# Kernel tuning notes

Measured on AMD Instinct MI355X. Metric: run time of the kernel, lower is better.

The kernel has to match this reference:

```python
import jax, jax.numpy as jnp
import numpy as np

GROUPS = 32
EPS = 1e-5


def setup_inputs() -> dict:
    key = jax.random.key(0)
    ks = jax.random.split(key, 4)
    B, C, H, W = 16, 512, 32, 32
    x = jax.random.normal(ks[0], (B, C, H, W), dtype=jnp.float32)
    gamma = jnp.ones((C,), jnp.float32)
    beta = jnp.zeros((C,), jnp.float32)
    # 1x1 convs as channel GEMMs; fan-in scaled init
    w_qkv = jax.random.normal(ks[1], (3 * C, C), dtype=jnp.float32) / np.sqrt(C)
    b_qkv = jnp.zeros((3 * C,), jnp.float32)
    w_proj = jax.random.normal(ks[2], (C, C), dtype=jnp.float32) / np.sqrt(C)
    b_proj = jnp.zeros((C,), jnp.float32)
    return {"x": x, "gamma": gamma, "beta": beta, "w_qkv": w_qkv,
            "b_qkv": b_qkv, "w_proj": w_proj, "b_proj": b_proj}


def _group_norm(x, gamma, beta):
    B, C, H, W = x.shape
    xg = x.reshape(B, GROUPS, C // GROUPS, H, W)
    mu = xg.mean(axis=(2, 3, 4), keepdims=True)
    var = xg.var(axis=(2, 3, 4), keepdims=True)
    xn = ((xg - mu) * jax.lax.rsqrt(var + EPS)).reshape(B, C, H, W)
    return xn * gamma[None, :, None, None] + beta[None, :, None, None]


def reference(x, gamma, beta, w_qkv, b_qkv, w_proj, b_proj):
    B, C, H, W = x.shape
    xn = _group_norm(x, gamma, beta)
    # 1x1 conv qkv: [B, 3C, H, W]
    qkv = jnp.einsum('oc,bchw->bohw', w_qkv, xn) + b_qkv[None, :, None, None]
    qkv = qkv.reshape(B, 3, C, H * W)
    q, k, v = qkv[:, 0], qkv[:, 1], qkv[:, 2]  # each [B, C, HW]
    scale = C ** (-0.5)
    # attn[b, i, j] = softmax_j( q[b,:,i] . k[b,:,j] * scale )
    attn = jax.nn.softmax(jnp.einsum('bci,bcj->bij', q, k) * scale, axis=-1)
    # out[b, c, i] = sum_j v[b,c,j] * attn[b,i,j]
    out = jnp.einsum('bcj,bij->bci', v, attn).reshape(B, C, H, W)
    proj = jnp.einsum('oc,bchw->bohw', w_proj, out) + b_proj[None, :, None, None]
    return x + proj
```

## Files before the change

kernel.cpp:

```cpp
#include <hip/hip_runtime.h>


typedef _Float16 f16;
typedef _Float16 f16x8 __attribute__((ext_vector_type(8)));
typedef _Float16 f16x4 __attribute__((ext_vector_type(4)));
typedef float fx4 __attribute__((ext_vector_type(4)));

__device__ __forceinline__ void gload16(const f16* g, f16* l) {
    __builtin_amdgcn_global_load_lds((const __attribute__((address_space(1))) void*)g,
                                     (__attribute__((address_space(3))) void*)l, 16, 0, 0);
}

__global__ __launch_bounds__(256)
void wconv_kernel(const float* __restrict__ w, f16* __restrict__ o, int n4)
{
    int i = blockIdx.x * 256 + threadIdx.x;
    if (i < n4) {
        float4 v = *(const float4*)(w + i * 4);
        f16x4 h;
        h[0] = (f16)v.x; h[1] = (f16)v.y; h[2] = (f16)v.z; h[3] = (f16)v.w;
        *(f16x4*)(o + i * 4) = h;
    }
}

__global__ __launch_bounds__(256)
void groupnorm_kernel(const float* __restrict__ x, const float* __restrict__ gamma,
                      const float* __restrict__ beta, f16* __restrict__ xnT)
{
    __shared__ float red[256], red2[256];
    __shared__ float mu_s, rs_s;
    __shared__ __align__(16) f16 T[16][520];
    const int blk = blockIdx.x;
    const int b = blk >> 5, g = blk & 31;
    const long base = (long)blk * (16 * 1024);
    const int tid = threadIdx.x;
    const float4* xv = (const float4*)(x + base);

    float s = 0.f, s2 = 0.f;
#pragma unroll
    for (int i = 0; i < 16; i++) {
        float4 v = xv[tid + i * 256];
        s  += v.x + v.y + v.z + v.w;
        s2 += v.x * v.x + v.y * v.y + v.z * v.z + v.w * v.w;
    }
    red[tid] = s; red2[tid] = s2;
    __syncthreads();
    for (int off = 128; off > 0; off >>= 1) {
        if (tid < off) { red[tid] += red[tid + off]; red2[tid] += red2[tid + off]; }
        __syncthreads();
    }
    if (tid == 0) {
        float mu = red[0] * (1.f / 16384.f);
        float var = red2[0] * (1.f / 16384.f) - mu * mu;
        mu_s = mu;
        rs_s = rsqrtf(var + 1e-5f);
    }
    __syncthreads();
    const float mu = mu_s, rs = rs_s;

    for (int h = 0; h < 2; h++) {
        if (h) __syncthreads();
#pragma unroll
        for (int i = 0; i < 8; i++) {
            int idx = tid + i * 256;
            int ch = idx >> 7;
            int p4 = idx & 127;
            float4 v = *(const float4*)(x + base + ch * 1024 + h * 512 + p4 * 4);
            float gm = gamma[g * 16 + ch] * rs;
            float bt = beta[g * 16 + ch] - mu * gm;
            f16x4 o;
            o[0] = (f16)(v.x * gm + bt);
            o[1] = (f16)(v.y * gm + bt);
            o[2] = (f16)(v.z * gm + bt);
            o[3] = (f16)(v.w * gm + bt);
            *(f16x4*)&T[ch][p4 * 4] = o;
        }
        __syncthreads();
#pragma unroll
        for (int i = 0; i < 4; i++) {
            int idx = tid + i * 256;
            int hw = idx >> 1;
            int half8 = (idx & 1) * 8;
            f16x8 o;
#pragma unroll
            for (int j = 0; j < 8; j++) o[j] = T[half8 + j][hw];
            long dst = ((long)b * 1024 + h * 512 + hw) * 512 + g * 16 + half8;
            *(f16x8*)(xnT + dst) = o;
        }
    }
}

__global__ __launch_bounds__(256)
void softmax_kernel(f16* __restrict__ S)
{
    const int wid = blockIdx.x * 4 + (threadIdx.x >> 6);
    const int lane = threadIdx.x & 63;
    f16* p = S + (long)wid * 1024 + lane * 16;
    f16x8 h0 = *(const f16x8*)p;
    f16x8 h1 = *(const f16x8*)(p + 8);
    float v[16];
#pragma unroll
    for (int i = 0; i < 8; i++) { v[i] = (float)h0[i]; v[8 + i] = (float)h1[i]; }
    float mx = v[0];
#pragma unroll
    for (int i = 1; i < 16; i++) mx = fmaxf(mx, v[i]);
    for (int off = 32; off > 0; off >>= 1) mx = fmaxf(mx, __shfl_xor(mx, off, 64));
    float sum = 0.f;
#pragma unroll
    for (int i = 0; i < 16; i++) { v[i] = __expf(v[i] - mx); sum += v[i]; }
    for (int off = 32; off > 0; off >>= 1) sum += __shfl_xor(sum, off, 64);
    const float inv = 1.f / sum;
#pragma unroll
    for (int i = 0; i < 8; i++) { h0[i] = (f16)(v[i] * inv); h1[i] = (f16)(v[8 + i] * inv); }
    *(f16x8*)p = h0;
    *(f16x8*)(p + 8) = h1;
}

template<int MODE>
__global__ __launch_bounds__(256)
void gemm_kernel(const f16* __restrict__ Ap, const f16* __restrict__ Bp,
                 void* __restrict__ Cp, f16* __restrict__ C2p,
                 const float* __restrict__ bias, const float* __restrict__ resid,
                 float alpha, int M, int N, int K, int lda, int ldb,
                 long sAb, long sBb, long sCb)
{
    __shared__ __align__(16) f16 As[2][128 * 32];
    __shared__ __align__(16) f16 Bs[2][128 * 32];

    const int b = blockIdx.z;
    const int m0 = blockIdx.y * 128, n0 = blockIdx.x * 128;
    const int tid = threadIdx.x;
    const int wave = tid >> 6, lane = tid & 63;
    const int quad = lane >> 4, l15 = lane & 15;
    const int wm = (wave >> 1) * 64, wn = (wave & 1) * 64;
    const int chunkoff = (quad ^ (l15 & 3)) * 8;

    const f16* Ag = Ap + (long)b * sAb;
    const f16* Bg = Bp + (long)b * sBb;

    const int si = lane >> 2;
    const int sj = lane & 3;

    const int R0 = wave * 32, R1 = wave * 32 + 16;
    const f16* agA0 = Ag + (long)(m0 + R0 + si) * lda + ((sj ^ ((R0 + si) & 3)) * 8);
    const f16* agA1 = Ag + (long)(m0 + R1 + si) * lda + ((sj ^ ((R1 + si) & 3)) * 8);
    const f16* agB0 = Bg + (long)(n0 + R0 + si) * ldb + ((sj ^ ((R0 + si) & 3)) * 8);
    const f16* agB1 = Bg + (long)(n0 + R1 + si) * ldb + ((sj ^ ((R1 + si) & 3)) * 8);

    fx4 acc[4][4] = {};

    const int nIter = K >> 5;
    gload16(agA0, &As[0][R0 * 32]);
    gload16(agA1, &As[0][R1 * 32]);
    gload16(agB0, &Bs[0][R0 * 32]);
    gload16(agB1, &Bs[0][R1 * 32]);

    for (int it = 0; it < nIter; ++it) {
        __syncthreads();
        const int cur = it & 1;
        if (it + 1 < nIter) {
            const int k = (it + 1) << 5;
            gload16(agA0 + k, &As[cur ^ 1][R0 * 32]);
            gload16(agA1 + k, &As[cur ^ 1][R1 * 32]);
            gload16(agB0 + k, &Bs[cur ^ 1][R0 * 32]);
            gload16(agB1 + k, &Bs[cur ^ 1][R1 * 32]);
        }
        f16x8 bf[4];
#pragma unroll
        for (int tn = 0; tn < 4; tn++)
            bf[tn] = *(const f16x8*)&Bs[cur][(wn + tn * 16 + l15) * 32 + chunkoff];
#pragma unroll
        for (int tm = 0; tm < 4; tm++) {
            f16x8 af = *(const f16x8*)&As[cur][(wm + tm * 16 + l15) * 32 + chunkoff];
#pragma unroll
            for (int tn = 0; tn < 4; tn++)
                acc[tm][tn] = __builtin_amdgcn_mfma_f32_16x16x32_f16(af, bf[tn], acc[tm][tn], 0, 0, 0);
        }
    }

    if (MODE == 1 && n0 >= 1024) {
#pragma unroll
        for (int tm = 0; tm < 4; tm++)
#pragma unroll
        for (int tn = 0; tn < 4; tn++) {
            int gc = n0 + wn + tn * 16 + l15;
            int gr0 = m0 + wm + tm * 16 + quad * 4;
            float bs = bias[gc];
            f16x4 o;
#pragma unroll
            for (int r = 0; r < 4; r++) o[r] = (f16)(acc[tm][tn][r] + bs);
            *(f16x4*)(C2p + (long)b * 524288 + (long)(gc - 1024) * 1024 + gr0) = o;
        }
        return;
    }
#pragma unroll
    for (int tm = 0; tm < 4; tm++)
#pragma unroll
    for (int tn = 0; tn < 4; tn++) {
        int gc = n0 + wn + tn * 16 + l15;
#pragma unroll
        for (int r = 0; r < 4; r++) {
            int gr = m0 + wm + tm * 16 + quad * 4 + r;
            float v = acc[tm][tn][r] * alpha;
            if (MODE == 1) {
                v += bias[gc];
                ((f16*)Cp)[(long)b * 1048576 + (long)gr * 1024 + gc] = (f16)v;
            } else if (MODE == 2) {
                v += bias[gr];
                long idx = (long)b * sCb + (long)gr * N + gc;
                v += resid[idx];
                ((float*)Cp)[idx] = v;
            } else {
                ((f16*)Cp)[(long)b * sCb + (long)gr * N + gc] = (f16)v;
            }
        }
    }
}

extern "C" void kernel_launch(void* const* d_in, const int* in_sizes, int n_in,
                              void* d_out, int out_size, void* d_ws, size_t ws_size,
                              hipStream_t stream)
{
    const float* x      = (const float*)d_in[0];
    const float* gamma  = (const float*)d_in[1];
    const float* beta   = (const float*)d_in[2];
    const float* w_qkv  = (const float*)d_in[3];
    const float* b_qkv  = (const float*)d_in[4];
    const float* w_proj = (const float*)d_in[5];
    const float* b_proj = (const float*)d_in[6];
    float* out = (float*)d_out;

    char* ws = (char*)d_ws;
    f16* xnT   = (f16*)(ws);
    f16* qkT   = (f16*)(ws + (16L << 20));
    f16* vbuf  = (f16*)(ws + (48L << 20));
    f16* S     = (f16*)(ws + (64L << 20));
    f16* aoutT = (f16*)(ws + (96L << 20));
    f16* wqkvh = S;
    f16* wprjh = xnT;

    wconv_kernel<<<768, 256, 0, stream>>>(w_qkv, wqkvh, 196608);

    groupnorm_kernel<<<512, 256, 0, stream>>>(x, gamma, beta, xnT);

    gemm_kernel<1><<<dim3(12, 8, 16), 256, 0, stream>>>(
        xnT, wqkvh, qkT, vbuf, b_qkv, nullptr, 1.0f,
        1024, 1536, 512, 512, 512,
        524288L, 0L, 0L);

    wconv_kernel<<<256, 256, 0, stream>>>(w_proj, wprjh, 65536);

    gemm_kernel<0><<<dim3(8, 8, 16), 256, 0, stream>>>(
        qkT, qkT + 512, S, nullptr, nullptr, nullptr, 0.04419417382415922f,
        1024, 1024, 512, 1024, 1024,
        1048576L, 1048576L, 1048576L);

    softmax_kernel<<<4096, 256, 0, stream>>>(S);

    gemm_kernel<0><<<dim3(4, 8, 16), 256, 0, stream>>>(
        S, vbuf, aoutT, nullptr, nullptr, nullptr, 1.0f,
        1024, 512, 1024, 1024, 1024,
        1048576L, 524288L, 524288L);

    gemm_kernel<2><<<dim3(8, 4, 16), 256, 0, stream>>>(
        wprjh, aoutT, out, nullptr, b_proj, x, 1.0f,
        512, 1024, 512, 512, 512,
        0L, 524288L, 524288L);
}
```

Measured before the change: 249.9 us.

## Use per-wave private LDS tiles with manual waitcnt pipelining in GEMM

```diff
diff --git a/kernel.cpp b/kernel.cpp
--- a/kernel.cpp
+++ b/kernel.cpp
@@ -5,6 +5,10 @@
 typedef _Float16 f16x8 __attribute__((ext_vector_type(8)));
 typedef _Float16 f16x4 __attribute__((ext_vector_type(4)));
 typedef float fx4 __attribute__((ext_vector_type(4)));
+
+#define WAIT_VM8   0x0F78
+#define WAIT_VM0   0x0F70
+#define WAIT_LGKM0 0xC07F
 
 __device__ __forceinline__ void gload16(const f16* g, f16* l) {
     __builtin_amdgcn_global_load_lds((const __attribute__((address_space(1))) void*)g,
@@ -29,17 +33,19 @@
 {
     __shared__ float red[256], red2[256];
     __shared__ float mu_s, rs_s;
-    __shared__ __align__(16) f16 T[16][520];
+    __shared__ __align__(16) f16 T[16][1040];
     const int blk = blockIdx.x;
     const int b = blk >> 5, g = blk & 31;
-    const long base = (long)blk * (16 * 1024);
+    const long base = (long)blk * 16384;
     const int tid = threadIdx.x;
     const float4* xv = (const float4*)(x + base);
 
+    float4 xr[16];
     float s = 0.f, s2 = 0.f;
 #pragma unroll
     for (int i = 0; i < 16; i++) {
         float4 v = xv[tid + i * 256];
+        xr[i] = v;
         s  += v.x + v.y + v.z + v.w;
         s2 += v.x * v.x + v.y * v.y + v.z * v.z + v.w * v.w;
     }
@@ -58,35 +64,29 @@
     __syncthreads();
     const float mu = mu_s, rs = rs_s;
 
-    for (int h = 0; h < 2; h++) {
-        if (h) __syncthreads();
-#pragma unroll
-        for (int i = 0; i < 8; i++) {
-            int idx = tid + i * 256;
-            int ch = idx >> 7;
-            int p4 = idx & 127;
-            float4 v = *(const float4*)(x + base + ch * 1024 + h * 512 + p4 * 4);
-            float gm = gamma[g * 16 + ch] * rs;
-            float bt = beta[g * 16 + ch] - mu * gm;
-            f16x4 o;
-            o[0] = (f16)(v.x * gm + bt);
-            o[1] = (f16)(v.y * gm + bt);
-            o[2] = (f16)(v.z * gm + bt);
-            o[3] = (f16)(v.w * gm + bt);
-            *(f16x4*)&T[ch][p4 * 4] = o;
-        }
-        __syncthreads();
-#pragma unroll
-        for (int i = 0; i < 4; i++) {
-            int idx = tid + i * 256;
-            int hw = idx >> 1;
-            int half8 = (idx & 1) * 8;
-            f16x8 o;
-#pragma unroll
-            for (int j = 0; j < 8; j++) o[j] = T[half8 + j][hw];
-            long dst = ((long)b * 1024 + h * 512 + hw) * 512 + g * 16 + half8;
-            *(f16x8*)(xnT + dst) = o;
-        }
+#pragma unroll
+    for (int i = 0; i < 16; i++) {
+        float gm = gamma[g * 16 + i] * rs;
+        float bt = beta[g * 16 + i] - mu * gm;
+        float4 v = xr[i];
+        f16x4 o;
+        o[0] = (f16)(v.x * gm + bt);
+        o[1] = (f16)(v.y * gm + bt);
+        o[2] = (f16)(v.z * gm + bt);
+        o[3] = (f16)(v.w * gm + bt);
+        *(f16x4*)&T[i][tid * 4] = o;
+    }
+    __syncthreads();
+#pragma unroll
+    for (int i = 0; i < 8; i++) {
+        int idx = tid + i * 256;
+        int hw = idx >> 1;
+        int half8 = (idx & 1) * 8;
+        f16x8 o;
+#pragma unroll
+        for (int j = 0; j < 8; j++) o[j] = T[half8 + j][hw];
+        long dst = ((long)b * 1024 + hw) * 512 + g * 16 + half8;
+        *(f16x8*)(xnT + dst) = o;
     }
 }
 
@@ -124,8 +124,7 @@
                  float alpha, int M, int N, int K, int lda, int ldb,
                  long sAb, long sBb, long sCb)
 {
-    __shared__ __align__(16) f16 As[2][128 * 32];
-    __shared__ __align__(16) f16 Bs[2][128 * 32];
+    __shared__ __align__(16) f16 lds[4][2][2][2048];
 
     const int b = blockIdx.z;
     const int m0 = blockIdx.y * 128, n0 = blockIdx.x * 128;
@@ -135,48 +134,64 @@
     const int wm = (wave >> 1) * 64, wn = (wave & 1) * 64;
     const int chunkoff = (quad ^ (l15 & 3)) * 8;
 
-    const f16* Ag = Ap + (long)b * sAb;
-    const f16* Bg = Bp + (long)b * sBb;
-
     const int si = lane >> 2;
     const int sj = lane & 3;
-
-    const int R0 = wave * 32, R1 = wave * 32 + 16;
-    const f16* agA0 = Ag + (long)(m0 + R0 + si) * lda + ((sj ^ ((R0 + si) & 3)) * 8);
-    const f16* agA1 = Ag + (long)(m0 + R1 + si) * lda + ((sj ^ ((R1 + si) & 3)) * 8);
-    const f16* agB0 = Bg + (long)(n0 + R0 + si) * ldb + ((sj ^ ((R0 + si) & 3)) * 8);
-    const f16* agB1 = Bg + (long)(n0 + R1 + si) * ldb + ((sj ^ ((R1 + si) & 3)) * 8);
+    const int sjx = (sj ^ (si & 3)) * 8;
+
+    const f16* Ag = Ap + (long)b * sAb + (long)(m0 + wm + si) * lda + sjx;
+    const f16* Bg = Bp + (long)b * sBb + (long)(n0 + wn + si) * ldb + sjx;
+
+    f16* ldsA = &lds[wave][0][0][0];
+    f16* ldsB = &lds[wave][1][0][0];
 
     fx4 acc[4][4] = {};
-
     const int nIter = K >> 5;
-    gload16(agA0, &As[0][R0 * 32]);
-    gload16(agA1, &As[0][R1 * 32]);
-    gload16(agB0, &Bs[0][R0 * 32]);
-    gload16(agB1, &Bs[0][R1 * 32]);
-
-    for (int it = 0; it < nIter; ++it) {
-        __syncthreads();
+
+#define STAGE(buf, kOff)                                                        \
+    { _Pragma("unroll")                                                          \
+      for (int s = 0; s < 4; s++) {                                              \
+          gload16(Ag + (kOff) + (s * 16) * lda, ldsA + (buf) * 2048 + s * 512);  \
+          gload16(Bg + (kOff) + (s * 16) * ldb, ldsB + (buf) * 2048 + s * 512);  \
+      } }
+
+    STAGE(0, 0)
+    STAGE(1, 32)
+
+    for (int it = 0; it < nIter - 1; ++it) {
         const int cur = it & 1;
-        if (it + 1 < nIter) {
-            const int k = (it + 1) << 5;
-            gload16(agA0 + k, &As[cur ^ 1][R0 * 32]);
-            gload16(agA1 + k, &As[cur ^ 1][R1 * 32]);
-            gload16(agB0 + k, &Bs[cur ^ 1][R0 * 32]);
-            gload16(agB1 + k, &Bs[cur ^ 1][R1 * 32]);
-        }
-        f16x8 bf[4];
-#pragma unroll
-        for (int tn = 0; tn < 4; tn++)
-            bf[tn] = *(const f16x8*)&Bs[cur][(wn + tn * 16 + l15) * 32 + chunkoff];
-#pragma unroll
-        for (int tm = 0; tm < 4; tm++) {
-            f16x8 af = *(const f16x8*)&As[cur][(wm + tm * 16 + l15) * 32 + chunkoff];
+        const f16* bA = ldsA + cur * 2048;
+        const f16* bB = ldsB + cur * 2048;
+        __builtin_amdgcn_s_waitcnt(WAIT_VM8);
+        f16x8 af[4], bf[4];
+#pragma unroll
+        for (int t = 0; t < 4; t++) af[t] = *(const f16x8*)&bA[(t * 16 + l15) * 32 + chunkoff];
+#pragma unroll
+        for (int t = 0; t < 4; t++) bf[t] = *(const f16x8*)&bB[(t * 16 + l15) * 32 + chunkoff];
+        __builtin_amdgcn_s_waitcnt(WAIT_LGKM0);
+        if (it + 2 < nIter) { STAGE(cur, (it + 2) << 5) }
+#pragma unroll
+        for (int tm = 0; tm < 4; tm++)
 #pragma unroll
             for (int tn = 0; tn < 4; tn++)
-                acc[tm][tn] = __builtin_amdgcn_mfma_f32_16x16x32_f16(af, bf[tn], acc[tm][tn], 0, 0, 0);
-        }
-    }
+                acc[tm][tn] = __builtin_amdgcn_mfma_f32_16x16x32_f16(af[tm], bf[tn], acc[tm][tn], 0, 0, 0);
+    }
+    {
+        const int cur = (nIter - 1) & 1;
+        const f16* bA = ldsA + cur * 2048;
+        const f16* bB = ldsB + cur * 2048;
+        __builtin_amdgcn_s_waitcnt(WAIT_VM0);
+        f16x8 af[4], bf[4];
+#pragma unroll
+        for (int t = 0; t < 4; t++) af[t] = *(const f16x8*)&bA[(t * 16 + l15) * 32 + chunkoff];
+#pragma unroll
+        for (int t = 0; t < 4; t++) bf[t] = *(const f16x8*)&bB[(t * 16 + l15) * 32 + chunkoff];
+#pragma unroll
+        for (int tm = 0; tm < 4; tm++)
+#pragma unroll
+            for (int tn = 0; tn < 4; tn++)
+                acc[tm][tn] = __builtin_amdgcn_mfma_f32_16x16x32_f16(af[tm], bf[tn], acc[tm][tn], 0, 0, 0);
+    }
+#undef STAGE
 
     if (MODE == 1 && n0 >= 1024) {
 #pragma unroll
```

After: 260.5 us. 4.2% more time.

## Fuse softmax into PV GEMM, remap block order, single-pass groupnorm

Applied to the files above, without the earlier changes.

```diff
diff --git a/kernel.cpp b/kernel.cpp
--- a/kernel.cpp
+++ b/kernel.cpp
@@ -5,6 +5,8 @@
 typedef _Float16 f16x8 __attribute__((ext_vector_type(8)));
 typedef _Float16 f16x4 __attribute__((ext_vector_type(4)));
 typedef float fx4 __attribute__((ext_vector_type(4)));
+
+#define LOG2E 1.44269504088896f
 
 __device__ __forceinline__ void gload16(const f16* g, f16* l) {
     __builtin_amdgcn_global_load_lds((const __attribute__((address_space(1))) void*)g,
@@ -29,17 +31,19 @@
 {
     __shared__ float red[256], red2[256];
     __shared__ float mu_s, rs_s;
-    __shared__ __align__(16) f16 T[16][520];
+    __shared__ __align__(16) f16 T[16][1040];
     const int blk = blockIdx.x;
     const int b = blk >> 5, g = blk & 31;
-    const long base = (long)blk * (16 * 1024);
+    const long base = (long)blk * 16384;
     const int tid = threadIdx.x;
     const float4* xv = (const float4*)(x + base);
 
+    float4 xr[16];
     float s = 0.f, s2 = 0.f;
 #pragma unroll
     for (int i = 0; i < 16; i++) {
         float4 v = xv[tid + i * 256];
+        xr[i] = v;
         s  += v.x + v.y + v.z + v.w;
         s2 += v.x * v.x + v.y * v.y + v.z * v.z + v.w * v.w;
     }
@@ -58,62 +62,30 @@
     __syncthreads();
     const float mu = mu_s, rs = rs_s;
 
-    for (int h = 0; h < 2; h++) {
-        if (h) __syncthreads();
-#pragma unroll
-        for (int i = 0; i < 8; i++) {
-            int idx = tid + i * 256;
-            int ch = idx >> 7;
-            int p4 = idx & 127;
-            float4 v = *(const float4*)(x + base + ch * 1024 + h * 512 + p4 * 4);
-            float gm = gamma[g * 16 + ch] * rs;
-            float bt = beta[g * 16 + ch] - mu * gm;
-            f16x4 o;
-            o[0] = (f16)(v.x * gm + bt);
-            o[1] = (f16)(v.y * gm + bt);
-            o[2] = (f16)(v.z * gm + bt);
-            o[3] = (f16)(v.w * gm + bt);
-            *(f16x4*)&T[ch][p4 * 4] = o;
-        }
-        __syncthreads();
-#pragma unroll
-        for (int i = 0; i < 4; i++) {
-            int idx = tid + i * 256;
-            int hw = idx >> 1;
-            int half8 = (idx & 1) * 8;
-            f16x8 o;
-#pragma unroll
-            for (int j = 0; j < 8; j++) o[j] = T[half8 + j][hw];
-            long dst = ((long)b * 1024 + h * 512 + hw) * 512 + g * 16 + half8;
-            *(f16x8*)(xnT + dst) = o;
-        }
-    }
-}
-
-__global__ __launch_bounds__(256)
-void softmax_kernel(f16* __restrict__ S)
-{
-    const int wid = blockIdx.x * 4 + (threadIdx.x >> 6);
-    const int lane = threadIdx.x & 63;
-    f16* p = S + (long)wid * 1024 + lane * 16;
-    f16x8 h0 = *(const f16x8*)p;
-    f16x8 h1 = *(const f16x8*)(p + 8);
-    float v[16];
-#pragma unroll
-    for (int i = 0; i < 8; i++) { v[i] = (float)h0[i]; v[8 + i] = (float)h1[i]; }
-    float mx = v[0];
-#pragma unroll
-    for (int i = 1; i < 16; i++) mx = fmaxf(mx, v[i]);
-    for (int off = 32; off > 0; off >>= 1) mx = fmaxf(mx, __shfl_xor(mx, off, 64));
-    float sum = 0.f;
-#pragma unroll
-    for (int i = 0; i < 16; i++) { v[i] = __expf(v[i] - mx); sum += v[i]; }
-    for (int off = 32; off > 0; off >>= 1) sum += __shfl_xor(sum, off, 64);
-    const float inv = 1.f / sum;
-#pragma unroll
-    for (int i = 0; i < 8; i++) { h0[i] = (f16)(v[i] * inv); h1[i] = (f16)(v[8 + i] * inv); }
-    *(f16x8*)p = h0;
-    *(f16x8*)(p + 8) = h1;
+#pragma unroll
+    for (int i = 0; i < 16; i++) {
+        float gm = gamma[g * 16 + i] * rs;
+        float bt = beta[g * 16 + i] - mu * gm;
+        float4 v = xr[i];
+        f16x4 o;
+        o[0] = (f16)(v.x * gm + bt);
+        o[1] = (f16)(v.y * gm + bt);
+        o[2] = (f16)(v.z * gm + bt);
+        o[3] = (f16)(v.w * gm + bt);
+        *(f16x4*)&T[i][tid * 4] = o;
+    }
+    __syncthreads();
+#pragma unroll
+    for (int i = 0; i < 8; i++) {
+        int idx = tid + i * 256;
+        int hw = idx >> 1;
+        int half8 = (idx & 1) * 8;
+        f16x8 o;
+#pragma unroll
+        for (int j = 0; j < 8; j++) o[j] = T[half8 + j][hw];
+        long dst = ((long)b * 1024 + hw) * 512 + g * 16 + half8;
+        *(f16x8*)(xnT + dst) = o;
+    }
 }
 
 template<int MODE>
@@ -126,9 +98,26 @@
 {
     __shared__ __align__(16) f16 As[2][128 * 32];
     __shared__ __align__(16) f16 Bs[2][128 * 32];
-
-    const int b = blockIdx.z;
-    const int m0 = blockIdx.y * 128, n0 = blockIdx.x * 128;
+    __shared__ float sm[128][2], sl[128][2];
+    __shared__ float ec_s[128], il_s[128];
+
+    const int linear = (blockIdx.z * gridDim.y + blockIdx.y) * gridDim.x + blockIdx.x;
+    int mIdx, nIdx, bIdx;
+    {
+        const int x7 = linear & 7, slot = linear >> 3;
+        if (MODE == 1) {
+            nIdx = slot >> 4; int t = x7 + 8 * (slot & 15); mIdx = t & 7; bIdx = t >> 3;
+        } else if (MODE == 0) {
+            bIdx = x7 + 8 * (slot >> 6); int mn = slot & 63; mIdx = mn >> 3; nIdx = mn & 7;
+        } else if (MODE == 3) {
+            bIdx = x7 + 8 * (slot >> 5); int mn = slot & 31; mIdx = mn >> 2; nIdx = mn & 3;
+        } else {
+            int t = x7 + 8 * (slot & 15); nIdx = t & 7; bIdx = t >> 3; mIdx = slot >> 4;
+        }
+    }
+    const int b = bIdx;
+    const int m0 = mIdx * 128, n0 = nIdx * 128;
+
     const int tid = threadIdx.x;
     const int wave = tid >> 6, lane = tid & 63;
     const int quad = lane >> 4, l15 = lane & 15;
@@ -138,9 +127,46 @@
     const f16* Ag = Ap + (long)b * sAb;
     const f16* Bg = Bp + (long)b * sBb;
 
-    const int si = lane >> 2;
-    const int sj = lane & 3;
-
+    float cf[4];
+    if (MODE == 3) {
+        const int r_loc = tid >> 1, half = tid & 1;
+        const f16* Srow = Ag + (long)(m0 + r_loc) * lda + half * 512;
+        float mx = -3.0e38f;
+        for (int ch = 0; ch < 64; ch += 8) {
+#pragma unroll
+            for (int u = 0; u < 8; u++) {
+                f16x8 v8 = *(const f16x8*)(Srow + (ch + u) * 8);
+#pragma unroll
+                for (int j = 0; j < 8; j++) mx = fmaxf(mx, (float)v8[j]);
+            }
+        }
+        float ssum = 0.f;
+        const float nc = -mx * LOG2E;
+        for (int ch = 0; ch < 64; ch += 8) {
+#pragma unroll
+            for (int u = 0; u < 8; u++) {
+                f16x8 v8 = *(const f16x8*)(Srow + (ch + u) * 8);
+#pragma unroll
+                for (int j = 0; j < 8; j++) ssum += exp2f(fmaf((float)v8[j], LOG2E, nc));
+            }
+        }
+        sm[r_loc][half] = mx;
+        sl[r_loc][half] = ssum;
+        __syncthreads();
+        if (half == 0) {
+            float m0h = sm[r_loc][0], m1h = sm[r_loc][1];
+            float mrow = fmaxf(m0h, m1h);
+            float l = sl[r_loc][0] * exp2f((m0h - mrow) * LOG2E)
+                    + sl[r_loc][1] * exp2f((m1h - mrow) * LOG2E);
+            ec_s[r_loc] = mrow * LOG2E;
+            il_s[r_loc] = 1.f / l;
+        }
+        __syncthreads();
+#pragma unroll
+        for (int tm = 0; tm < 4; tm++) cf[tm] = ec_s[wm + tm * 16 + l15];
+    }
+
+    const int si = lane >> 2, sj = lane & 3;
     const int R0 = wave * 32, R1 = wave * 32 + 16;
     const f16* agA0 = Ag + (long)(m0 + R0 + si) * lda + ((sj ^ ((R0 + si) & 3)) * 8);
     const f16* agA1 = Ag + (long)(m0 + R1 + si) * lda + ((sj ^ ((R1 + si) & 3)) * 8);
@@ -148,23 +174,20 @@
     const f16* agB1 = Bg + (long)(n0 + R1 + si) * ldb + ((sj ^ ((R1 + si) & 3)) * 8);
 
     fx4 acc[4][4] = {};
-
     const int nIter = K >> 5;
-    gload16(agA0, &As[0][R0 * 32]);
-    gload16(agA1, &As[0][R1 * 32]);
-    gload16(agB0, &Bs[0][R0 * 32]);
-    gload16(agB1, &Bs[0][R1 * 32]);
+
+#define STAGE(buf, kOff)                                          \
+    { gload16(agA0 + (kOff), &As[buf][R0 * 32]);                   \
+      gload16(agA1 + (kOff), &As[buf][R1 * 32]);                   \
+      gload16(agB0 + (kOff), &Bs[buf][R0 * 32]);                   \
+      gload16(agB1 + (kOff), &Bs[buf][R1 * 32]); }
+
+    STAGE(0, 0)
 
     for (int it = 0; it < nIter; ++it) {
         __syncthreads();
         const int cur = it & 1;
-        if (it + 1 < nIter) {
-            const int k = (it + 1) << 5;
-            gload16(agA0 + k, &As[cur ^ 1][R0 * 32]);
-            gload16(agA1 + k, &As[cur ^ 1][R1 * 32]);
-            gload16(agB0 + k, &Bs[cur ^ 1][R0 * 32]);
-            gload16(agB1 + k, &Bs[cur ^ 1][R1 * 32]);
-        }
+        if (it + 1 < nIter) { STAGE(cur ^ 1, (it + 1) << 5) }
         f16x8 bf[4];
 #pragma unroll
         for (int tn = 0; tn < 4; tn++)
@@ -172,11 +195,19 @@
 #pragma unroll
         for (int tm = 0; tm < 4; tm++) {
             f16x8 af = *(const f16x8*)&As[cur][(wm + tm * 16 + l15) * 32 + chunkoff];
+            if (MODE == 3) {
+                f16x8 pf;
+#pragma unroll
+                for (int j = 0; j < 8; j++)
+                    pf[j] = (f16)exp2f(fmaf((float)af[j], LOG2E, -cf[tm]));
+                af = pf;
+            }
 #pragma unroll
             for (int tn = 0; tn < 4; tn++)
                 acc[tm][tn] = __builtin_amdgcn_mfma_f32_16x16x32_f16(af, bf[tn], acc[tm][tn], 0, 0, 0);
         }
     }
+#undef STAGE
 
     if (MODE == 1 && n0 >= 1024) {
 #pragma unroll
@@ -193,6 +224,13 @@
         }
         return;
     }
+    float ilr[4][4];
+    if (MODE == 3) {
+#pragma unroll
+        for (int tm = 0; tm < 4; tm++)
+#pragma unroll
+            for (int r = 0; r < 4; r++) ilr[tm][r] = il_s[wm + tm * 16 + quad * 4 + r];
+    }
 #pragma unroll
     for (int tm = 0; tm < 4; tm++)
 #pragma unroll
@@ -201,17 +239,21 @@
 #pragma unroll
         for (int r = 0; r < 4; r++) {
             int gr = m0 + wm + tm * 16 + quad * 4 + r;
-            float v = acc[tm][tn][r] * alpha;
-            if (MODE == 1) {
+            float v = acc[tm][tn][r];
+            if (MODE == 0) {
+                v *= alpha;
+                ((f16*)Cp)[(long)b * sCb + (long)gr * N + gc] = (f16)v;
+            } else if (MODE == 3) {
+                v *= ilr[tm][r];
+                ((f16*)Cp)[(long)b * sCb + (long)gr * N + gc] = (f16)v;
+            } else if (MODE == 1) {
                 v += bias[gc];
                 ((f16*)Cp)[(long)b * 1048576 + (long)gr * 1024 + gc] = (f16)v;
-            } else if (MODE == 2) {
+            } else {
                 v += bias[gr];
                 long idx = (long)b * sCb + (long)gr * N + gc;
                 v += resid[idx];
                 ((float*)Cp)[idx] = v;
-            } else {
-                ((f16*)Cp)[(long)b * sCb + (long)gr * N + gc] = (f16)v;
             }
         }
     }
@@ -255,9 +297,7 @@
         1024, 1024, 512, 1024, 1024,
         1048576L, 1048576L, 1048576L);
 
-    softmax_kernel<<<4096, 256, 0, stream>>>(S);
-
-    gemm_kernel<0><<<dim3(4, 8, 16), 256, 0, stream>>>(
+    gemm_kernel<3><<<dim3(4, 8, 16), 256, 0, stream>>>(
         S, vbuf, aoutT, nullptr, nullptr, nullptr, 1.0f,
         1024, 512, 1024, 1024, 1024,
         1048576L, 524288L, 524288L);
```

New measurement: 277.9 us. 1.11x slower.

## Halve GEMM M-tile, remap blocks across batches for XCD locality, register-cache groupnorm input

Applied to the files above, without the earlier changes.

```diff
diff --git a/kernel.cpp b/kernel.cpp
--- a/kernel.cpp
+++ b/kernel.cpp
@@ -29,17 +29,19 @@
 {
     __shared__ float red[256], red2[256];
     __shared__ float mu_s, rs_s;
-    __shared__ __align__(16) f16 T[16][520];
+    __shared__ __align__(16) f16 T[16][1040];
     const int blk = blockIdx.x;
     const int b = blk >> 5, g = blk & 31;
-    const long base = (long)blk * (16 * 1024);
+    const long base = (long)blk * 16384;
     const int tid = threadIdx.x;
     const float4* xv = (const float4*)(x + base);
 
+    float4 xr[16];
     float s = 0.f, s2 = 0.f;
 #pragma unroll
     for (int i = 0; i < 16; i++) {
         float4 v = xv[tid + i * 256];
+        xr[i] = v;
         s  += v.x + v.y + v.z + v.w;
         s2 += v.x * v.x + v.y * v.y + v.z * v.z + v.w * v.w;
     }
@@ -58,35 +60,29 @@
     __syncthreads();
     const float mu = mu_s, rs = rs_s;
 
-    for (int h = 0; h < 2; h++) {
-        if (h) __syncthreads();
-#pragma unroll
-        for (int i = 0; i < 8; i++) {
-            int idx = tid + i * 256;
-            int ch = idx >> 7;
-            int p4 = idx & 127;
-            float4 v = *(const float4*)(x + base + ch * 1024 + h * 512 + p4 * 4);
-            float gm = gamma[g * 16 + ch] * rs;
-            float bt = beta[g * 16 + ch] - mu * gm;
-            f16x4 o;
-            o[0] = (f16)(v.x * gm + bt);
-            o[1] = (f16)(v.y * gm + bt);
-            o[2] = (f16)(v.z * gm + bt);
-            o[3] = (f16)(v.w * gm + bt);
-            *(f16x4*)&T[ch][p4 * 4] = o;
-        }
-        __syncthreads();
-#pragma unroll
-        for (int i = 0; i < 4; i++) {
-            int idx = tid + i * 256;
-            int hw = idx >> 1;
-            int half8 = (idx & 1) * 8;
-            f16x8 o;
-#pragma unroll
-            for (int j = 0; j < 8; j++) o[j] = T[half8 + j][hw];
-            long dst = ((long)b * 1024 + h * 512 + hw) * 512 + g * 16 + half8;
-            *(f16x8*)(xnT + dst) = o;
-        }
+#pragma unroll
+    for (int i = 0; i < 16; i++) {
+        float gm = gamma[g * 16 + i] * rs;
+        float bt = beta[g * 16 + i] - mu * gm;
+        float4 v = xr[i];
+        f16x4 o;
+        o[0] = (f16)(v.x * gm + bt);
+        o[1] = (f16)(v.y * gm + bt);
+        o[2] = (f16)(v.z * gm + bt);
+        o[3] = (f16)(v.w * gm + bt);
+        *(f16x4*)&T[i][tid * 4] = o;
+    }
+    __syncthreads();
+#pragma unroll
+    for (int i = 0; i < 8; i++) {
+        int idx = tid + i * 256;
+        int hw = idx >> 1;
+        int half8 = (idx & 1) * 8;
+        f16x8 o;
+#pragma unroll
+        for (int j = 0; j < 8; j++) o[j] = T[half8 + j][hw];
+        long dst = ((long)b * 1024 + hw) * 512 + g * 16 + half8;
+        *(f16x8*)(xnT + dst) = o;
     }
 }
 
@@ -124,63 +120,63 @@
                  float alpha, int M, int N, int K, int lda, int ldb,
                  long sAb, long sBb, long sCb)
 {
-    __shared__ __align__(16) f16 As[2][128 * 32];
+    __shared__ __align__(16) f16 As[2][64 * 32];
     __shared__ __align__(16) f16 Bs[2][128 * 32];
 
-    const int b = blockIdx.z;
-    const int m0 = blockIdx.y * 128, n0 = blockIdx.x * 128;
+    const int linear = (blockIdx.z * gridDim.y + blockIdx.y) * gridDim.x + blockIdx.x;
+    const int nTiles = gridDim.x, nm = gridDim.x * gridDim.y;
+    const int x7 = linear & 7, slot = linear >> 3;
+    const int b = x7 + 8 * (slot / nm);
+    const int rem = slot % nm;
+    const int mIdx = rem / nTiles, nIdx = rem % nTiles;
+    const int m0 = mIdx * 64, n0 = nIdx * 128;
+
     const int tid = threadIdx.x;
     const int wave = tid >> 6, lane = tid & 63;
     const int quad = lane >> 4, l15 = lane & 15;
-    const int wm = (wave >> 1) * 64, wn = (wave & 1) * 64;
+    const int wm = (wave >> 1) * 32, wn = (wave & 1) * 64;
     const int chunkoff = (quad ^ (l15 & 3)) * 8;
 
     const f16* Ag = Ap + (long)b * sAb;
     const f16* Bg = Bp + (long)b * sBb;
 
-    const int si = lane >> 2;
-    const int sj = lane & 3;
-
-    const int R0 = wave * 32, R1 = wave * 32 + 16;
-    const f16* agA0 = Ag + (long)(m0 + R0 + si) * lda + ((sj ^ ((R0 + si) & 3)) * 8);
-    const f16* agA1 = Ag + (long)(m0 + R1 + si) * lda + ((sj ^ ((R1 + si) & 3)) * 8);
-    const f16* agB0 = Bg + (long)(n0 + R0 + si) * ldb + ((sj ^ ((R0 + si) & 3)) * 8);
-    const f16* agB1 = Bg + (long)(n0 + R1 + si) * ldb + ((sj ^ ((R1 + si) & 3)) * 8);
-
-    fx4 acc[4][4] = {};
-
+    const int si = lane >> 2, sj = lane & 3;
+    const int RA = wave * 16, RB0 = wave * 32, RB1 = wave * 32 + 16;
+    const f16* agA  = Ag + (long)(m0 + RA  + si) * lda + ((sj ^ ((RA  + si) & 3)) * 8);
+    const f16* agB0 = Bg + (long)(n0 + RB0 + si) * ldb + ((sj ^ ((RB0 + si) & 3)) * 8);
+    const f16* agB1 = Bg + (long)(n0 + RB1 + si) * ldb + ((sj ^ ((RB1 + si) & 3)) * 8);
+
+    fx4 acc[2][4] = {};
     const int nIter = K >> 5;
-    gload16(agA0, &As[0][R0 * 32]);
-    gload16(agA1, &As[0][R1 * 32]);
-    gload16(agB0, &Bs[0][R0 * 32]);
-    gload16(agB1, &Bs[0][R1 * 32]);
+
+#define STAGE(buf, kOff)                                          \
+    { gload16(agA  + (kOff), &As[buf][RA  * 32]);                  \
+      gload16(agB0 + (kOff), &Bs[buf][RB0 * 32]);                  \
+      gload16(agB1 + (kOff), &Bs[buf][RB1 * 32]); }
+
+    STAGE(0, 0)
 
     for (int it = 0; it < nIter; ++it) {
         __syncthreads();
         const int cur = it & 1;
-        if (it + 1 < nIter) {
-            const int k = (it + 1) << 5;
-            gload16(agA0 + k, &As[cur ^ 1][R0 * 32]);
-            gload16(agA1 + k, &As[cur ^ 1][R1 * 32]);
-            gload16(agB0 + k, &Bs[cur ^ 1][R0 * 32]);
-            gload16(agB1 + k, &Bs[cur ^ 1][R1 * 32]);
-        }
+        if (it + 1 < nIter) { STAGE(cur ^ 1, (it + 1) << 5) }
         f16x8 bf[4];
 #pragma unroll
         for (int tn = 0; tn < 4; tn++)
             bf[tn] = *(const f16x8*)&Bs[cur][(wn + tn * 16 + l15) * 32 + chunkoff];
 #pragma unroll
-        for (int tm = 0; tm < 4; tm++) {
+        for (int tm = 0; tm < 2; tm++) {
             f16x8 af = *(const f16x8*)&As[cur][(wm + tm * 16 + l15) * 32 + chunkoff];
 #pragma unroll
             for (int tn = 0; tn < 4; tn++)
                 acc[tm][tn] = __builtin_amdgcn_mfma_f32_16x16x32_f16(af, bf[tn], acc[tm][tn], 0, 0, 0);
         }
     }
+#undef STAGE
 
     if (MODE == 1 && n0 >= 1024) {
 #pragma unroll
-        for (int tm = 0; tm < 4; tm++)
+        for (int tm = 0; tm < 2; tm++)
 #pragma unroll
         for (int tn = 0; tn < 4; tn++) {
             int gc = n0 + wn + tn * 16 + l15;
@@ -194,24 +190,25 @@
         return;
     }
 #pragma unroll
-    for (int tm = 0; tm < 4; tm++)
+    for (int tm = 0; tm < 2; tm++)
 #pragma unroll
     for (int tn = 0; tn < 4; tn++) {
         int gc = n0 + wn + tn * 16 + l15;
 #pragma unroll
         for (int r = 0; r < 4; r++) {
             int gr = m0 + wm + tm * 16 + quad * 4 + r;
-            float v = acc[tm][tn][r] * alpha;
-            if (MODE == 1) {
+            float v = acc[tm][tn][r];
+            if (MODE == 0) {
+                v *= alpha;
+                ((f16*)Cp)[(long)b * sCb + (long)gr * N + gc] = (f16)v;
+            } else if (MODE == 1) {
                 v += bias[gc];
                 ((f16*)Cp)[(long)b * 1048576 + (long)gr * 1024 + gc] = (f16)v;
-            } else if (MODE == 2) {
+            } else {
                 v += bias[gr];
                 long idx = (long)b * sCb + (long)gr * N + gc;
                 v += resid[idx];
                 ((float*)Cp)[idx] = v;
-            } else {
-                ((f16*)Cp)[(long)b * sCb + (long)gr * N + gc] = (f16)v;
             }
         }
     }
@@ -243,26 +240,26 @@
 
     groupnorm_kernel<<<512, 256, 0, stream>>>(x, gamma, beta, xnT);
 
-    gemm_kernel<1><<<dim3(12, 8, 16), 256, 0, stream>>>(
+    gemm_kernel<1><<<dim3(12, 16, 16), 256, 0, stream>>>(
         xnT, wqkvh, qkT, vbuf, b_qkv, nullptr, 1.0f,
         1024, 1536, 512, 512, 512,
         524288L, 0L, 0L);
 
     wconv_kernel<<<256, 256, 0, stream>>>(w_proj, wprjh, 65536);
 
-    gemm_kernel<0><<<dim3(8, 8, 16), 256, 0, stream>>>(
+    gemm_kernel<0><<<dim3(8, 16, 16), 256, 0, stream>>>(
         qkT, qkT + 512, S, nullptr, nullptr, nullptr, 0.04419417382415922f,
         1024, 1024, 512, 1024, 1024,
         1048576L, 1048576L, 1048576L);
 
     softmax_kernel<<<4096, 256, 0, stream>>>(S);
 
-    gemm_kernel<0><<<dim3(4, 8, 16), 256, 0, stream>>>(
+    gemm_kernel<0><<<dim3(4, 16, 16), 256, 0, stream>>>(
         S, vbuf, aoutT, nullptr, nullptr, nullptr, 1.0f,
         1024, 512, 1024, 1024, 1024,
         1048576L, 524288L, 524288L);
 
-    gemm_kernel<2><<<dim3(8, 4, 16), 256, 0, stream>>>(
+    gemm_kernel<2><<<dim3(8, 8, 16), 256, 0, stream>>>(
         wprjh, aoutT, out, nullptr, b_proj, x, 1.0f,
         512, 1024, 512, 512, 512,
         0L, 524288L, 524288L);
```

After: 239.2 us. 1.04x faster.
